# Performance work log

Hardware: AMD Instinct MI355X
Metric: run time of the kernel (lower is better)

The kernel has to match this reference:

```python
import jax, jax.numpy as jnp
import numpy as np

N_WIN, P, C = 2048, 64, 256      # total windows, tokens per window (8x8 partition), channels
M_SEL, KEEP, REAL = 1536, 48, 40 # selected windows, topk tokens kept per window, real (non-padded)
H, DH = 8, 32                    # heads, dim_head
EPS = 1e-5


def _ln(x, g, b):
    mu = jnp.mean(x, axis=-1, keepdims=True)
    v = jnp.mean(jnp.square(x - mu), axis=-1, keepdims=True)
    return (x - mu) * jax.lax.rsqrt(v + EPS) * g + b


def setup_inputs() -> dict:
    key = jax.random.key(0)
    ks = jax.random.split(key, 6)
    rng = np.random.default_rng(0)
    # distinct selected windows
    index_window = jnp.asarray(np.sort(rng.choice(N_WIN, size=M_SEL, replace=False)), jnp.int32)
    # per selected window: 48 distinct token positions out of 64; first 40 real, last 8 padded
    pos = np.argsort(rng.random((M_SEL, P)), axis=1)[:, :KEEP]
    tok = np.arange(M_SEL)[:, None] * P + pos           # flat rows into (M*P, C)
    index_token = jnp.asarray(tok.reshape(-1), jnp.int32)
    asy_index = jnp.asarray(tok[:, :REAL].reshape(-1), jnp.int32)
    padding_index = jnp.asarray(tok[:, REAL:].reshape(-1), jnp.int32)
    w = lambda k, s: jax.random.normal(k, s, jnp.float32) * 0.02
    return {
        "x": jax.random.normal(ks[0], (N_WIN, P, C), jnp.float32),
        "qkv_w": w(ks[1], (C, 3 * C)), "qkv_b": jnp.zeros((3 * C,), jnp.float32),
        "proj_w": w(ks[2], (C, C)), "proj_b": jnp.zeros((C,), jnp.float32),
        "norm1_g": jnp.ones((C,), jnp.float32), "norm1_b": jnp.zeros((C,), jnp.float32),
        "norm2_g": jnp.ones((C,), jnp.float32), "norm2_b": jnp.zeros((C,), jnp.float32),
        "ls1_g": jnp.full((C,), 1e-5, jnp.float32), "ls2_g": jnp.full((C,), 1e-5, jnp.float32),
        "mlp_w1": w(ks[3], (C, 4 * C)), "mlp_b1": jnp.zeros((4 * C,), jnp.float32),
        "mlp_w2": w(ks[4], (4 * C, C)), "mlp_b2": jnp.zeros((C,), jnp.float32),
        "index_window": index_window, "index_token": index_token,
        "padding_index": padding_index, "asy_index": asy_index,
        "M": M_SEL,
    }


def reference(x, qkv_w, qkv_b, proj_w, proj_b, norm1_g, norm1_b, norm2_g, norm2_b,
              ls1_g, ls2_g, mlp_w1, mlp_b1, mlp_w2, mlp_b2,
              index_window, index_token, padding_index, asy_index, M):
    scale = DH ** -0.5
    x1 = _ln(x, norm1_g, norm1_b)                       # norm1 over all windows (N,P,C)
    X = x1
    XX = x1[index_window].reshape(-1, C)                # gather selected windows -> (M*P, C)
    XX = XX.at[asy_index].set(_ln(XX[asy_index], norm2_g, norm2_b))
    shortcut = XX[asy_index]
    xt = XX[index_token].reshape(M, KEEP, C)            # gather kept tokens per window
    qkv = (xt @ qkv_w + qkv_b).reshape(M, KEEP, H, 3 * DH).transpose(0, 2, 1, 3)
    q, k, v = jnp.split(qkv, 3, axis=-1)                # each (M,H,KEEP,DH)
    attn = jnp.einsum('mhqd,mhkd->mhqk', q, k) * scale  # (M,H,Q,K)
    # scatter scores into full map keyed by KEY token row, mask padded keys, gather back
    am = attn.transpose(0, 3, 2, 1).reshape(M * KEEP, KEEP, H)
    attn_map = jnp.zeros((M * P, KEEP, H), attn.dtype)
    attn_map = attn_map.at[index_token].set(am)
    attn_map = attn_map.at[padding_index].set(-10000.0)
    attn = attn_map[index_token].reshape(M, KEEP, KEEP, H).transpose(0, 3, 2, 1)
    attn = jax.nn.softmax(attn, axis=-1)
    out = jnp.einsum('mhqk,mhkd->mhqd', attn, v).transpose(0, 2, 1, 3).reshape(M, KEEP, C)
    out = out @ proj_w + proj_b
    XX = XX.at[index_token].set(out.reshape(-1, C))
    xa = shortcut + XX[asy_index] * ls1_g               # residual + LayerScale
    hdn = jax.nn.gelu(xa @ mlp_w1 + mlp_b1, approximate=False)
    xa = xa + (hdn @ mlp_w2 + mlp_b2) * ls2_g           # (enable_CB=False path)
    XX = XX.at[asy_index].set(xa)
    Xw = X[index_window].reshape(-1, C)
    XX = XX.at[padding_index].set(Xw[padding_index])    # restore padded rows
    X = X.at[index_window].set(XX.reshape(M, P, C))     # scatter windows back
    return X
```

## Files before the change

### kernel.cpp

```cpp
#include <hip/hip_runtime.h>

typedef __attribute__((ext_vector_type(8))) short bf16x8;
typedef __attribute__((ext_vector_type(4))) float f32x4;
typedef unsigned short u16;
typedef unsigned int u32;

#define NWIN 2048
#define P 64
#define C 256
#define MSEL 1536
#define KEEP 48
#define REAL 40
#define H 8
#define DH 32
#define MROWS (MSEL * REAL)

#define OFF_WQKVT  0
#define OFF_PROJT  196608
#define OFF_W1T    262144
#define OFF_W2T    524288
#define OFF_A      786432
#define OFF_QKV    16515072
#define OFF_ATTNO  63700992
#define OFF_XA     79429632
#define OFF_H      16515072

__device__ __forceinline__ u16 f2bf(float f) {
    u32 u = __float_as_uint(f);
    u += 0x7FFF + ((u >> 16) & 1);
    return (u16)(u >> 16);
}
__device__ __forceinline__ float bf2f(u16 h) { return __uint_as_float(((u32)h) << 16); }

__global__ __launch_bounds__(256) void prep_weights(const float* __restrict__ qkv_w,
                                                    const float* __restrict__ proj_w,
                                                    const float* __restrict__ w1,
                                                    const float* __restrict__ w2,
                                                    u16* __restrict__ ws) {
    int i = blockIdx.x * 256 + threadIdx.x;
    float v; int o;
    if (i < 196608) {
        int n = i >> 8, k = i & 255; v = qkv_w[k * 768 + n]; o = OFF_WQKVT + i;
    } else if (i < 262144) {
        int j = i - 196608; int n = j >> 8, k = j & 255; v = proj_w[k * 256 + n]; o = i;
    } else if (i < 524288) {
        int j = i - 262144; int n = j >> 8, k = j & 255; v = w1[k * 1024 + n]; o = i;
    } else {
        int j = i - 524288; int n = j >> 10, k = j & 1023; v = w2[k * 256 + n]; o = i;
    }
    ws[o] = f2bf(v);
}

__global__ __launch_bounds__(256) void ln1_kernel(const float* __restrict__ x,
                                                  const float* __restrict__ g,
                                                  const float* __restrict__ b,
                                                  float* __restrict__ out) {
    int row = blockIdx.x * 4 + (threadIdx.x >> 6);
    int l = threadIdx.x & 63;
    const float4 v = *(const float4*)(x + (size_t)row * C + l * 4);
    float s = v.x + v.y + v.z + v.w;
    float q = v.x * v.x + v.y * v.y + v.z * v.z + v.w * v.w;
    #pragma unroll
    for (int m = 1; m < 64; m <<= 1) { s += __shfl_xor(s, m); q += __shfl_xor(q, m); }
    float mu = s * (1.0f / C);
    float var = q * (1.0f / C) - mu * mu;
    float rs = rsqrtf(var + 1e-5f);
    float4 gg = *(const float4*)(g + l * 4);
    float4 bb = *(const float4*)(b + l * 4);
    float4 o;
    o.x = (v.x - mu) * rs * gg.x + bb.x;
    o.y = (v.y - mu) * rs * gg.y + bb.y;
    o.z = (v.z - mu) * rs * gg.z + bb.z;
    o.w = (v.w - mu) * rs * gg.w + bb.w;
    *(float4*)(out + (size_t)row * C + l * 4) = o;
}

__global__ __launch_bounds__(256) void ln2_kernel(const float* __restrict__ ln1,
                                                  const float* __restrict__ g,
                                                  const float* __restrict__ b,
                                                  const int* __restrict__ asy,
                                                  const int* __restrict__ iwin,
                                                  u16* __restrict__ A) {
    int r = blockIdx.x * 4 + (threadIdx.x >> 6);
    int l = threadIdx.x & 63;
    int flat = asy[r];
    int m = flat >> 6, p = flat & 63;
    int w = iwin[m];
    const float4 v = *(const float4*)(ln1 + ((size_t)w * P + p) * C + l * 4);
    float s = v.x + v.y + v.z + v.w;
    float q = v.x * v.x + v.y * v.y + v.z * v.z + v.w * v.w;
    #pragma unroll
    for (int mm = 1; mm < 64; mm <<= 1) { s += __shfl_xor(s, mm); q += __shfl_xor(q, mm); }
    float mu = s * (1.0f / C);
    float var = q * (1.0f / C) - mu * mu;
    float rs = rsqrtf(var + 1e-5f);
    float4 gg = *(const float4*)(g + l * 4);
    float4 bb = *(const float4*)(b + l * 4);
    ushort4 o;
    o.x = f2bf((v.x - mu) * rs * gg.x + bb.x);
    o.y = f2bf((v.y - mu) * rs * gg.y + bb.y);
    o.z = f2bf((v.z - mu) * rs * gg.z + bb.z);
    o.w = f2bf((v.w - mu) * rs * gg.w + bb.w);
    *(ushort4*)(A + (size_t)r * C + l * 4) = o;
}

template <int N, int K, class Epi>
__global__ __launch_bounds__(256) void gemm_bt(const u16* __restrict__ A,
                                               const u16* __restrict__ B, Epi epi) {
    constexpr int NB = N / 128;
    int bid = blockIdx.x;
    int bm = bid / NB, bn = bid % NB;
    __shared__ u16 lA[128 * 40], lB[128 * 40];
    int t = threadIdx.x;
    int l = t & 63, w = t >> 6;
    int wr = w >> 1, wc = w & 1;
    int l15 = l & 15, g4 = l >> 4;

    f32x4 acc[4][4];
    #pragma unroll
    for (int a = 0; a < 4; a++)
        #pragma unroll
        for (int bb = 0; bb < 4; bb++)
            #pragma unroll
            for (int i = 0; i < 4; i++) acc[a][bb][i] = 0.0f;

    int sr = t >> 1, sh = (t & 1) * 16;
    const u16* gA = A + (size_t)(bm * 128 + sr) * K + sh;
    const u16* gB = B + (size_t)(bn * 128 + sr) * K + sh;
    u16* wA = lA + sr * 40 + sh;
    u16* wB = lB + sr * 40 + sh;

    for (int k0 = 0; k0 < K; k0 += 32) {
        uint4 a0 = *(const uint4*)(gA + k0);
        uint4 a1 = *(const uint4*)(gA + k0 + 8);
        uint4 b0 = *(const uint4*)(gB + k0);
        uint4 b1 = *(const uint4*)(gB + k0 + 8);
        __syncthreads();
        *(uint4*)wA = a0; *(uint4*)(wA + 8) = a1;
        *(uint4*)wB = b0; *(uint4*)(wB + 8) = b1;
        __syncthreads();
        bf16x8 af[4], bf[4];
        #pragma unroll
        for (int mt = 0; mt < 4; mt++)
            af[mt] = *(const bf16x8*)(lA + (wr * 64 + mt * 16 + l15) * 40 + g4 * 8);
        #pragma unroll
        for (int nt = 0; nt < 4; nt++)
            bf[nt] = *(const bf16x8*)(lB + (wc * 64 + nt * 16 + l15) * 40 + g4 * 8);
        #pragma unroll
        for (int mt = 0; mt < 4; mt++)
            #pragma unroll
            for (int nt = 0; nt < 4; nt++)
                acc[mt][nt] = __builtin_amdgcn_mfma_f32_16x16x32_bf16(af[mt], bf[nt], acc[mt][nt], 0, 0, 0);
    }
    int orow = bm * 128 + wr * 64, ocol = bn * 128 + wc * 64;
    #pragma unroll
    for (int mt = 0; mt < 4; mt++)
        #pragma unroll
        for (int nt = 0; nt < 4; nt++)
            #pragma unroll
            for (int rg = 0; rg < 4; rg++)
                epi(orow + mt * 16 + g4 * 4 + rg, ocol + nt * 16 + l15, acc[mt][nt][rg]);
}

struct EpiQKV {
    const float* bias; u16* out;
    __device__ void operator()(int r, int c, float v) const {
        out[(size_t)r * 768 + c] = f2bf(v + bias[c]);
    }
};
struct EpiProj {
    const float* bias; const float* ls1; const u16* Abuf; u16* xa;
    __device__ void operator()(int r, int c, float v) const {
        float val = bf2f(Abuf[(size_t)r * 256 + c]) + (v + bias[c]) * ls1[c];
        xa[(size_t)r * 256 + c] = f2bf(val);
    }
};
struct EpiMLP1 {
    const float* bias; u16* h;
    __device__ void operator()(int r, int c, float v) const {
        float x = v + bias[c];
        float gl = 0.5f * x * (1.0f + erff(x * 0.70710678118654752f));
        h[(size_t)r * 1024 + c] = f2bf(gl);
    }
};
struct EpiMLP2 {
    const float* bias; const float* ls2; const u16* xa;
    const int* asy; const int* iwin; float* out;
    __device__ void operator()(int r, int c, float v) const {
        float val = bf2f(xa[(size_t)r * 256 + c]) + (v + bias[c]) * ls2[c];
        int flat = asy[r];
        int m = flat >> 6, p = flat & 63;
        int wdw = iwin[m];
        out[((size_t)wdw * P + p) * C + c] = val;
    }
};

__global__ __launch_bounds__(256) void attn_kernel(const u16* __restrict__ QKV,
                                                   u16* __restrict__ out) {
    __shared__ u16 lds[4 * (48 * 80 + 32 * 80)];
    int m = blockIdx.x;
    int t = threadIdx.x, l = t & 63, w = t >> 6;
    int l15 = l & 15, g4 = l >> 4;
    u16* Pb = lds + w * (48 * 80 + 32 * 80);
    u16* Vt = Pb + 48 * 80;

    u32* z = (u32*)Pb;
    for (int i = l; i < (48 * 80 + 32 * 80) / 2; i += 64) z[i] = 0;

    const float scale = 0.17677669529663687f;

    for (int hh = 0; hh < 2; hh++) {
        int h = w + hh * 4;
        const u16* base = QKV + (size_t)m * REAL * 768 + h * 96;

        for (int idx = l; idx < REAL * DH; idx += 64) {
            int kk = idx >> 5, d = idx & 31;
            Vt[d * 80 + kk] = base[(size_t)kk * 768 + 64 + d];
        }

        bf16x8 zf;
        #pragma unroll
        for (int i = 0; i < 8; i++) zf[i] = 0;
        bf16x8 qf[3], kf[3];
        #pragma unroll
        for (int mt = 0; mt < 3; mt++) {
            int q = mt * 16 + l15;
            qf[mt] = (q < REAL) ? *(const bf16x8*)(base + (size_t)q * 768 + g4 * 8) : zf;
        }
        #pragma unroll
        for (int nt = 0; nt < 3; nt++) {
            int kk = nt * 16 + l15;
            kf[nt] = (kk < REAL) ? *(const bf16x8*)(base + (size_t)kk * 768 + 32 + g4 * 8) : zf;
        }
        f32x4 s[3][3];
        #pragma unroll
        for (int a = 0; a < 3; a++)
            #pragma unroll
            for (int bb = 0; bb < 3; bb++)
                #pragma unroll
                for (int i = 0; i < 4; i++) s[a][bb][i] = 0.0f;
        #pragma unroll
        for (int mt = 0; mt < 3; mt++)
            #pragma unroll
            for (int nt = 0; nt < 3; nt++)
                s[mt][nt] = __builtin_amdgcn_mfma_f32_16x16x32_bf16(qf[mt], kf[nt], s[mt][nt], 0, 0, 0);

        #pragma unroll
        for (int mt = 0; mt < 3; mt++) {
            #pragma unroll
            for (int rg = 0; rg < 4; rg++) {
                float v0 = s[mt][0][rg] * scale;
                float v1 = s[mt][1][rg] * scale;
                float v2 = s[mt][2][rg] * scale;
                bool k2ok = (32 + l15) < REAL;
                float mx = fmaxf(fmaxf(v0, v1), k2ok ? v2 : -1e30f);
                #pragma unroll
                for (int xm = 1; xm < 16; xm <<= 1) mx = fmaxf(mx, __shfl_xor(mx, xm));
                float e0 = __expf(v0 - mx);
                float e1 = __expf(v1 - mx);
                float e2 = k2ok ? __expf(v2 - mx) : 0.0f;
                float sm = e0 + e1 + e2;
                #pragma unroll
                for (int xm = 1; xm < 16; xm <<= 1) sm += __shfl_xor(sm, xm);
                float inv = 1.0f / sm;
                int q = mt * 16 + g4 * 4 + rg;
                Pb[q * 80 + l15]      = f2bf(e0 * inv);
                Pb[q * 80 + 16 + l15] = f2bf(e1 * inv);
                Pb[q * 80 + 32 + l15] = f2bf(e2 * inv);
            }
        }

        f32x4 o[3][2];
        #pragma unroll
        for (int a = 0; a < 3; a++)
            #pragma unroll
            for (int bb = 0; bb < 2; bb++)
                #pragma unroll
                for (int i = 0; i < 4; i++) o[a][bb][i] = 0.0f;
        #pragma unroll
        for (int kt = 0; kt < 2; kt++) {
            bf16x8 pf[3], vf[2];
            #pragma unroll
            for (int mt = 0; mt < 3; mt++)
                pf[mt] = *(const bf16x8*)(Pb + (mt * 16 + l15) * 80 + kt * 32 + g4 * 8);
            #pragma unroll
            for (int nt = 0; nt < 2; nt++)
                vf[nt] = *(const bf16x8*)(Vt + (nt * 16 + l15) * 80 + kt * 32 + g4 * 8);
            #pragma unroll
            for (int mt = 0; mt < 3; mt++)
                #pragma unroll
                for (int nt = 0; nt < 2; nt++)
                    o[mt][nt] = __builtin_amdgcn_mfma_f32_16x16x32_bf16(pf[mt], vf[nt], o[mt][nt], 0, 0, 0);
        }
        #pragma unroll
        for (int mt = 0; mt < 3; mt++)
            #pragma unroll
            for (int nt = 0; nt < 2; nt++)
                #pragma unroll
                for (int rg = 0; rg < 4; rg++) {
                    int q = mt * 16 + g4 * 4 + rg;
                    if (q < REAL)
                        out[((size_t)m * REAL + q) * C + h * DH + nt * 16 + l15] = f2bf(o[mt][nt][rg]);
                }
    }
}

extern "C" void kernel_launch(void* const* d_in, const int* in_sizes, int n_in,
                              void* d_out, int out_size, void* d_ws, size_t ws_size,
                              hipStream_t stream) {
    const float* x      = (const float*)d_in[0];
    const float* qkv_w  = (const float*)d_in[1];
    const float* qkv_b  = (const float*)d_in[2];
    const float* proj_w = (const float*)d_in[3];
    const float* proj_b = (const float*)d_in[4];
    const float* n1g    = (const float*)d_in[5];
    const float* n1b    = (const float*)d_in[6];
    const float* n2g    = (const float*)d_in[7];
    const float* n2b    = (const float*)d_in[8];
    const float* ls1    = (const float*)d_in[9];
    const float* ls2    = (const float*)d_in[10];
    const float* w1     = (const float*)d_in[11];
    const float* b1     = (const float*)d_in[12];
    const float* w2     = (const float*)d_in[13];
    const float* b2     = (const float*)d_in[14];
    const int*   iwin   = (const int*)d_in[15];
    const int*   asy    = (const int*)d_in[18];
    float* out = (float*)d_out;
    u16* ws = (u16*)d_ws;

    u16* WqkvT = ws + OFF_WQKVT;
    u16* ProjT = ws + OFF_PROJT;
    u16* W1T   = ws + OFF_W1T;
    u16* W2T   = ws + OFF_W2T;
    u16* Abuf  = ws + OFF_A;
    u16* QKV   = ws + OFF_QKV;
    u16* AttnO = ws + OFF_ATTNO;
    u16* XA    = ws + OFF_XA;
    u16* Hbuf  = ws + OFF_H;

    prep_weights<<<3072, 256, 0, stream>>>(qkv_w, proj_w, w1, w2, ws);
    ln1_kernel<<<(NWIN * P) / 4, 256, 0, stream>>>(x, n1g, n1b, out);
    ln2_kernel<<<MROWS / 4, 256, 0, stream>>>(out, n2g, n2b, asy, iwin, Abuf);
    gemm_bt<768, 256, EpiQKV><<<(MROWS / 128) * 6, 256, 0, stream>>>(Abuf, WqkvT, EpiQKV{qkv_b, QKV});
    attn_kernel<<<MSEL, 256, 0, stream>>>(QKV, AttnO);
    gemm_bt<256, 256, EpiProj><<<(MROWS / 128) * 2, 256, 0, stream>>>(AttnO, ProjT, EpiProj{proj_b, ls1, Abuf, XA});
    gemm_bt<1024, 256, EpiMLP1><<<(MROWS / 128) * 8, 256, 0, stream>>>(XA, W1T, EpiMLP1{b1, Hbuf});
    gemm_bt<256, 1024, EpiMLP2><<<(MROWS / 128) * 2, 256, 0, stream>>>(Hbuf, W2T, EpiMLP2{b2, ls2, XA, asy, iwin, out});
}
```

Before: 591.1 us.

## Use direct global-to-LDS loads with XOR swizzle, K=64 tiles, XCD-aware block remap

Rewrites the GEMM main loop to load A and B tiles straight into LDS with global_load_lds. It doubles the K step to 64 and applies an XOR swizzle to avoid LDS bank conflicts. Block IDs are remapped so consecutive tiles land on the same XCD, which should improve L2 reuse. The attention kernel now reads V with 16-byte vector loads instead of scalar loads. The changes aim to cut register staging, LDS conflicts and global-load inefficiency, but the loop still stalls at a barrier each iteration with no double buffering, and the remap assumes the block count divides by 8.

```diff
diff --git a/kernel.cpp b/kernel.cpp
--- a/kernel.cpp
+++ b/kernel.cpp
@@ -106,15 +106,18 @@
 
 template <int N, int K, class Epi>
 __global__ __launch_bounds__(256) void gemm_bt(const u16* __restrict__ A,
-                                               const u16* __restrict__ B, Epi epi) {
+                                               const u16* __restrict__ B, Epi epi,
+                                               int chunk) {
     constexpr int NB = N / 128;
     int bid = blockIdx.x;
+    bid = (bid & 7) * chunk + (bid >> 3);
     int bm = bid / NB, bn = bid % NB;
-    __shared__ u16 lA[128 * 40], lB[128 * 40];
+    __shared__ u16 lA[128 * 64], lB[128 * 64];
     int t = threadIdx.x;
     int l = t & 63, w = t >> 6;
     int wr = w >> 1, wc = w & 1;
     int l15 = l & 15, g4 = l >> 4;
+    int xr = l15 & 7;
 
     f32x4 acc[4][4];
     #pragma unroll
@@ -124,33 +127,41 @@
             #pragma unroll
             for (int i = 0; i < 4; i++) acc[a][bb][i] = 0.0f;
 
-    int sr = t >> 1, sh = (t & 1) * 16;
-    const u16* gA = A + (size_t)(bm * 128 + sr) * K + sh;
-    const u16* gB = B + (size_t)(bn * 128 + sr) * K + sh;
-    u16* wA = lA + sr * 40 + sh;
-    u16* wB = lB + sr * 40 + sh;
-
-    for (int k0 = 0; k0 < K; k0 += 32) {
-        uint4 a0 = *(const uint4*)(gA + k0);
-        uint4 a1 = *(const uint4*)(gA + k0 + 8);
-        uint4 b0 = *(const uint4*)(gB + k0);
-        uint4 b1 = *(const uint4*)(gB + k0 + 8);
+    int rbase = w * 32 + (l >> 3);
+    int cg = (l & 7) ^ (l >> 3);
+    const u16* gA = A + (size_t)(bm * 128 + rbase) * K + cg * 8;
+    const u16* gB = B + (size_t)(bn * 128 + rbase) * K + cg * 8;
+
+    for (int k0 = 0; k0 < K; k0 += 64) {
         __syncthreads();
-        *(uint4*)wA = a0; *(uint4*)(wA + 8) = a1;
-        *(uint4*)wB = b0; *(uint4*)(wB + 8) = b1;
+        #pragma unroll
+        for (int j = 0; j < 4; j++)
+            __builtin_amdgcn_global_load_lds(
+                (const __attribute__((address_space(1))) u32*)(gA + (size_t)j * 8 * K + k0),
+                (__attribute__((address_space(3))) u32*)(lA + w * 2048 + j * 512), 16, 0, 0);
+        #pragma unroll
+        for (int j = 0; j < 4; j++)
+            __builtin_amdgcn_global_load_lds(
+                (const __attribute__((address_space(1))) u32*)(gB + (size_t)j * 8 * K + k0),
+                (__attribute__((address_space(3))) u32*)(lB + w * 2048 + j * 512), 16, 0, 0);
         __syncthreads();
-        bf16x8 af[4], bf[4];
-        #pragma unroll
-        for (int mt = 0; mt < 4; mt++)
-            af[mt] = *(const bf16x8*)(lA + (wr * 64 + mt * 16 + l15) * 40 + g4 * 8);
-        #pragma unroll
-        for (int nt = 0; nt < 4; nt++)
-            bf[nt] = *(const bf16x8*)(lB + (wc * 64 + nt * 16 + l15) * 40 + g4 * 8);
-        #pragma unroll
-        for (int mt = 0; mt < 4; mt++)
+        #pragma unroll
+        for (int kk = 0; kk < 2; kk++) {
+            bf16x8 af[4], bfr[4];
+            #pragma unroll
+            for (int mt = 0; mt < 4; mt++)
+                af[mt] = *(const bf16x8*)(lA + (wr * 64 + mt * 16 + l15) * 64
+                                             + ((kk * 4 + g4) ^ xr) * 8);
             #pragma unroll
             for (int nt = 0; nt < 4; nt++)
-                acc[mt][nt] = __builtin_amdgcn_mfma_f32_16x16x32_bf16(af[mt], bf[nt], acc[mt][nt], 0, 0, 0);
+                bfr[nt] = *(const bf16x8*)(lB + (wc * 64 + nt * 16 + l15) * 64
+                                              + ((kk * 4 + g4) ^ xr) * 8);
+            #pragma unroll
+            for (int mt = 0; mt < 4; mt++)
+                #pragma unroll
+                for (int nt = 0; nt < 4; nt++)
+                    acc[mt][nt] = __builtin_amdgcn_mfma_f32_16x16x32_bf16(af[mt], bfr[nt], acc[mt][nt], 0, 0, 0);
+        }
     }
     int orow = bm * 128 + wr * 64, ocol = bn * 128 + wc * 64;
     #pragma unroll
@@ -213,9 +224,11 @@
         int h = w + hh * 4;
         const u16* base = QKV + (size_t)m * REAL * 768 + h * 96;
 
-        for (int idx = l; idx < REAL * DH; idx += 64) {
-            int kk = idx >> 5, d = idx & 31;
-            Vt[d * 80 + kk] = base[(size_t)kk * 768 + 64 + d];
+        for (int i = l; i < REAL * 4; i += 64) {
+            int kk = i >> 2, dg = i & 3;
+            bf16x8 vv = *(const bf16x8*)(base + (size_t)kk * 768 + 64 + dg * 8);
+            #pragma unroll
+            for (int j = 0; j < 8; j++) Vt[(dg * 8 + j) * 80 + kk] = vv[j];
         }
 
         bf16x8 zf;
@@ -341,9 +354,21 @@
     prep_weights<<<3072, 256, 0, stream>>>(qkv_w, proj_w, w1, w2, ws);
     ln1_kernel<<<(NWIN * P) / 4, 256, 0, stream>>>(x, n1g, n1b, out);
     ln2_kernel<<<MROWS / 4, 256, 0, stream>>>(out, n2g, n2b, asy, iwin, Abuf);
-    gemm_bt<768, 256, EpiQKV><<<(MROWS / 128) * 6, 256, 0, stream>>>(Abuf, WqkvT, EpiQKV{qkv_b, QKV});
+    {
+        int nwg = (MROWS / 128) * 6;
+        gemm_bt<768, 256, EpiQKV><<<nwg, 256, 0, stream>>>(Abuf, WqkvT, EpiQKV{qkv_b, QKV}, nwg / 8);
+    }
     attn_kernel<<<MSEL, 256, 0, stream>>>(QKV, AttnO);
-    gemm_bt<256, 256, EpiProj><<<(MROWS / 128) * 2, 256, 0, stream>>>(AttnO, ProjT, EpiProj{proj_b, ls1, Abuf, XA});
-    gemm_bt<1024, 256, EpiMLP1><<<(MROWS / 128) * 8, 256, 0, stream>>>(XA, W1T, EpiMLP1{b1, Hbuf});
-    gemm_bt<256, 1024, EpiMLP2><<<(MROWS / 128) * 2, 256, 0, stream>>>(Hbuf, W2T, EpiMLP2{b2, ls2, XA, asy, iwin, out});
-}
+    {
+        int nwg = (MROWS / 128) * 2;
+        gemm_bt<256, 256, EpiProj><<<nwg, 256, 0, stream>>>(AttnO, ProjT, EpiProj{proj_b, ls1, Abuf, XA}, nwg / 8);
+    }
+    {
+        int nwg = (MROWS / 128) * 8;
+        gemm_bt<1024, 256, EpiMLP1><<<nwg, 256, 0, stream>>>(XA, W1T, EpiMLP1{b1, Hbuf}, nwg / 8);
+    }
+    {
+        int nwg = (MROWS / 128) * 2;
+        gemm_bt<256, 1024, EpiMLP2><<<nwg, 256, 0, stream>>>(Hbuf, W2T, EpiMLP2{b2, ls2, XA, asy, iwin, out}, nwg / 8);
+    }
+}
```

New measurement: 517.7 us. -12.4%, faster.
